# Optimization experiments

Hardware: AMD Instinct MI355X
Metric: run time of the kernel (lower is better)

## Reference

```python
import jax, jax.numpy as jnp
import numpy as np
from jax import lax

B, N, C = 256, 256, 192
HEADS = 6
HD = C // HEADS
WIN = 16
AGENT = 49
POOL = 7            # int(agent_num ** 0.5)
SCALE = HD ** -0.5


def _pool_matrix(inn, out):
    # PyTorch AdaptiveAvgPool2d bin edges: start=floor(i*inn/out), end=ceil((i+1)*inn/out)
    P = np.zeros((out, inn), np.float32)
    for i in range(out):
        s = (i * inn) // out
        e = -(((-(i + 1)) * inn) // out)
        P[i, s:e] = 1.0 / (e - s)
    return jnp.asarray(P)

_P = _pool_matrix(WIN, POOL)  # (7, 16) adaptive-avg-pool operator


def _resize_bilinear(x, out_h, out_w):
    # matches F.interpolate(mode='bilinear', align_corners=False)
    H, W = x.shape[-2], x.shape[-1]
    def idx(out, inn):
        s = (jnp.arange(out, dtype=jnp.float32) + 0.5) * (inn / out) - 0.5
        s = jnp.maximum(s, 0.0)
        i0 = jnp.minimum(jnp.floor(s).astype(jnp.int32), inn - 1)
        i1 = jnp.minimum(i0 + 1, inn - 1)
        return i0, i1, s - i0.astype(jnp.float32)
    h0, h1, th = idx(out_h, H)
    w0, w1, tw = idx(out_w, W)
    xh = x[..., h0, :] * (1.0 - th)[:, None] + x[..., h1, :] * th[:, None]
    return xh[..., :, w0] * (1.0 - tw) + xh[..., :, w1] * tw


def setup_inputs() -> dict:
    key = jax.random.key(0)
    ks = jax.random.split(key, 18)
    lin = lambda k: jax.random.normal(k, (C, C), jnp.float32) * 0.02
    zc = jnp.zeros((C,), jnp.float32)
    tn = lambda k, shp: jax.random.normal(k, shp, jnp.float32) * 0.02
    return {
        "x_F1": jax.random.normal(ks[0], (B, N, C), jnp.float32),
        "x_C2": jax.random.normal(ks[1], (B, N, C), jnp.float32),
        "x_C1": jax.random.normal(ks[2], (B, N, C), jnp.float32),
        "Wq": lin(ks[3]), "bq": zc,
        "Wk": lin(ks[4]), "bk": zc,
        "Wv": lin(ks[5]), "bv": zc,
        "Wa1": lin(ks[6]), "ba1": zc,
        "Wa2": lin(ks[7]), "ba2": zc,
        "an_bias": tn(ks[8], (HEADS, AGENT, 7, 7)),
        "na_bias": tn(ks[9], (HEADS, AGENT, 7, 7)),
        "ah_bias": tn(ks[10], (1, HEADS, AGENT, WIN, 1)),
        "aw_bias": tn(ks[11], (1, HEADS, AGENT, 1, WIN)),
        "ha_bias": tn(ks[12], (1, HEADS, WIN, 1, AGENT)),
        "wa_bias": tn(ks[13], (1, HEADS, 1, WIN, AGENT)),
        "dwc_w": tn(ks[14], (C, 1, 3, 3)),
        "dwc_b": zc,
        "Wp": lin(ks[15]), "bp": zc,
    }


def reference(x_F1, x_C2, x_C1, Wq, bq, Wk, bk, Wv, bv, Wa1, ba1, Wa2, ba2,
              an_bias, na_bias, ah_bias, aw_bias, ha_bias, wa_bias,
              dwc_w, dwc_b, Wp, bp):
    b, n, c = x_F1.shape
    h = w = WIN
    q = x_F1 @ Wq.T + bq
    k = (x_F1 + x_C2 - x_C1) @ Wk.T + bk
    v = (x_C2 - x_C1) @ Wv.T + bv
    # agent tokens: linear -> adaptive avg pool 16x16 -> 7x7 -> (b, 49, c)
    a1 = (x_C1 @ Wa1.T + ba1).reshape(b, h, w, c)
    a1 = jnp.einsum('ph,bhwc,qw->bpqc', _P, a1, _P).reshape(b, AGENT, c)
    a2 = (x_C2 @ Wa2.T + ba2).reshape(b, h, w, c)
    a2 = jnp.einsum('ph,bhwc,qw->bpqc', _P, a2, _P).reshape(b, AGENT, c)
    qh = q.reshape(b, n, HEADS, HD).transpose(0, 2, 1, 3)
    kh = k.reshape(b, n, HEADS, HD).transpose(0, 2, 1, 3)
    vh = v.reshape(b, n, HEADS, HD).transpose(0, 2, 1, 3)
    a1h = a1.reshape(b, AGENT, HEADS, HD).transpose(0, 2, 1, 3)
    a2h = a2.reshape(b, AGENT, HEADS, HD).transpose(0, 2, 1, 3)
    # stage 1: agent <- k/v attention, bias = interp(an_bias) + (ah+aw)
    pb = (_resize_bilinear(an_bias, h, w).reshape(1, HEADS, AGENT, n)
          + (ah_bias + aw_bias).reshape(1, HEADS, AGENT, n))
    attn2 = jax.nn.softmax(SCALE * jnp.einsum('bhad,bhnd->bhan', a2h, kh) + pb, axis=-1)
    agent_v = jnp.einsum('bhan,bhnd->bhad', attn2, vh)
    # stage 2: query <- agent attention, bias = interp(na_bias)^T + (ha+wa)
    ab = (jnp.swapaxes(_resize_bilinear(na_bias, h, w).reshape(HEADS, AGENT, n), -1, -2)[None]
          + (ha_bias + wa_bias).reshape(1, HEADS, n, AGENT))
    q_attn = jax.nn.softmax(SCALE * jnp.einsum('bhnd,bhad->bhna', qh, a1h) + ab, axis=-1)
    x = jnp.einsum('bhna,bhad->bhnd', q_attn, agent_v).transpose(0, 2, 1, 3).reshape(b, n, c)
    # depthwise 3x3 conv on q as spatial map
    q_img = q.reshape(b, h, w, c).transpose(0, 3, 1, 2)
    dw = lax.conv_general_dilated(q_img, dwc_w, (1, 1), ((1, 1), (1, 1)),
                                  feature_group_count=c,
                                  dimension_numbers=('NCHW', 'OIHW', 'NCHW'))
    dw = dw + dwc_b.reshape(1, c, 1, 1)
    x = x + dw.transpose(0, 2, 3, 1).reshape(b, n, c)
    return x @ Wp.T + bp
```

## Files before the change

kernel.cpp:

```cpp
#include <hip/hip_runtime.h>

typedef __bf16 bf16;
typedef __bf16 bf16x8 __attribute__((ext_vector_type(8)));
typedef float  f32x4  __attribute__((ext_vector_type(4)));

#define DEVI __device__ __forceinline__

static constexpr int   BATCH = 256;
static constexpr int   SEQ   = 256;
static constexpr int   CH    = 192;
static constexpr int   NH    = 6;
static constexpr int   AG    = 49;
static constexpr float QK_SCALE = 0.17677669529663687f;

__device__ constexpr int   PPN[16]  = {1,1,2,1,2,1,2,1,1,2,1,2,1,2,1,1};
__device__ constexpr int   PPB0[16] = {0,0,0,1,1,2,2,3,3,3,4,4,5,5,6,6};
__device__ constexpr int   PPB1[16] = {0,0,1,0,2,0,3,0,0,4,0,5,0,6,0,0};
__device__ constexpr float PPW0[16] = {1.f/3.f,1.f/3.f,1.f/3.f,1.f/3.f,1.f/3.f,1.f/3.f,1.f/3.f,0.25f,0.25f,0.25f,
                                       1.f/3.f,1.f/3.f,1.f/3.f,1.f/3.f,1.f/3.f,1.f/3.f};
__device__ constexpr float PPW1[16] = {0.f,0.f,1.f/3.f,0.f,1.f/3.f,0.f,0.25f,0.f,0.f,1.f/3.f,
                                       0.f,1.f/3.f,0.f,1.f/3.f,0.f,0.f};

DEVI float bilin7(const float* m, int i, int j) {
  float sh = (i + 0.5f) * 0.4375f - 0.5f; sh = sh < 0.f ? 0.f : sh;
  float sw = (j + 0.5f) * 0.4375f - 0.5f; sw = sw < 0.f ? 0.f : sw;
  int i0 = (int)sh; if (i0 > 6) i0 = 6;
  int j0 = (int)sw; if (j0 > 6) j0 = 6;
  int i1 = i0 + 1;  if (i1 > 6) i1 = 6;
  int j1 = j0 + 1;  if (j1 > 6) j1 = 6;
  float th = sh - (float)i0, tw = sw - (float)j0;
  float v00 = m[i0*7 + j0], v01 = m[i0*7 + j1];
  float v10 = m[i1*7 + j0], v11 = m[i1*7 + j1];
  return (v00*(1.f-tw) + v01*tw)*(1.f-th) + (v10*(1.f-tw) + v11*tw)*th;
}

__global__ void k_prep(const float* Wq, const float* Wk, const float* Wv,
                       const float* Wa1, const float* Wa2, const float* Wp,
                       const float* an_bias, const float* na_bias,
                       const float* ah_bias, const float* aw_bias,
                       const float* ha_bias, const float* wa_bias,
                       bf16* wsW, float* pb, float* ab, bf16* a1, bf16* a2) {
  int gid = blockIdx.x * 256 + threadIdx.x;
  if (gid < 221184) {
    int mi = gid / 36864, r = gid - mi * 36864;
    const float* W = (mi == 0 ? Wq : mi == 1 ? Wk : mi == 2 ? Wv :
                      mi == 3 ? Wa1 : mi == 4 ? Wa2 : Wp);
    wsW[gid] = (bf16)W[r];
  } else if (gid < 296448) {
    int r = gid - 221184;
    int n = r & 255, ha = r >> 8;
    int i = n >> 4, j = n & 15;
    float val = bilin7(an_bias + (size_t)ha * 49, i, j)
              + ah_bias[ha * 16 + i] + aw_bias[ha * 16 + j];
    pb[r] = val;
  } else if (gid < 371712) {
    int r = gid - 296448;
    int a = r % 49, hn = r / 49;
    int n = hn & 255, hh = hn >> 8;
    int i = n >> 4, j = n & 15;
    float val = bilin7(na_bias + (size_t)(hh * 49 + a) * 49, i, j)
              + ha_bias[(hh * 16 + i) * 49 + a] + wa_bias[(hh * 16 + j) * 49 + a];
    ab[r] = val;
  } else if (gid < 396288) {
    int r = gid - 371712;
    if (r < 12288) a1[(size_t)12544 * CH + r] = (bf16)0.f;
    else           a2[(size_t)12544 * CH + (r - 12288)] = (bf16)0.f;
  }
}

__global__ __launch_bounds__(768, 3) void k_gemm3(
    const float* xF1, const float* xC2, const float* xC1,
    const bf16* wsW, const float* bq, const float* bk, const float* bv,
    bf16* qO, bf16* kO, bf16* vO) {
  __shared__ bf16 sT[3][128][72] __attribute__((aligned(16)));
  const int tid = threadIdx.x, lane = tid & 63, wid = tid >> 6;
  const int l15 = lane & 15, lg = lane >> 4;
  const int job = wid >> 2, quad = wid & 3;
  const int wr = quad >> 1, wc = quad & 1;
  const int m0 = blockIdx.x * 128;

  const bf16*  Wj   = wsW + job * 36864;
  const float* bias = (job == 0) ? bq : (job == 1) ? bk : bv;
  bf16*        outp = (job == 0) ? qO : (job == 1) ? kO : vO;

  f32x4 acc[4][6];
  #pragma unroll
  for (int a = 0; a < 4; ++a)
    #pragma unroll
    for (int b2 = 0; b2 < 6; ++b2) acc[a][b2] = f32x4{0.f, 0.f, 0.f, 0.f};

  const int srow = tid >> 2, qtr = tid & 3;
  const size_t rb = (size_t)(m0 + srow) * CH;

  for (int ks = 0; ks < 3; ++ks) {
    const int k0 = ks * 64;
    if (tid < 512) {
      const int cb = k0 + qtr * 16;
      float4 F[4], A2[4], A1[4];
      const float4* pF = (const float4*)(xF1 + rb + cb);
      const float4* p2 = (const float4*)(xC2 + rb + cb);
      const float4* p1 = (const float4*)(xC1 + rb + cb);
      #pragma unroll
      for (int i = 0; i < 4; ++i) { F[i] = pF[i]; A2[i] = p2[i]; A1[i] = p1[i]; }
      const float* ff = (const float*)F;
      const float* f2 = (const float*)A2;
      const float* f1 = (const float*)A1;
      bf16x8 tq[2], tk[2], tv[2];
      #pragma unroll
      for (int e = 0; e < 16; ++e) {
        const int w = e >> 3, l = e & 7;
        const float xf = ff[e], x2 = f2[e], x1 = f1[e];
        tq[w][l] = (bf16)xf;
        tk[w][l] = (bf16)(xf + x2 - x1);
        tv[w][l] = (bf16)(x2 - x1);
      }
      *(bf16x8*)&sT[0][srow][qtr * 16]     = tq[0];
      *(bf16x8*)&sT[0][srow][qtr * 16 + 8] = tq[1];
      *(bf16x8*)&sT[1][srow][qtr * 16]     = tk[0];
      *(bf16x8*)&sT[1][srow][qtr * 16 + 8] = tk[1];
      *(bf16x8*)&sT[2][srow][qtr * 16]     = tv[0];
      *(bf16x8*)&sT[2][srow][qtr * 16 + 8] = tv[1];
    }
    __syncthreads();
    #pragma unroll
    for (int kk = 0; kk < 64; kk += 32) {
      bf16x8 af[4];
      #pragma unroll
      for (int rt = 0; rt < 4; ++rt)
        af[rt] = *(const bf16x8*)&sT[job][64 * wr + 16 * rt + l15][kk + 8 * lg];
      #pragma unroll
      for (int ct = 0; ct < 6; ++ct) {
        const int ncol = 96 * wc + 16 * ct + l15;
        bf16x8 bfr = *(const bf16x8*)&Wj[(size_t)ncol * CH + k0 + kk + 8 * lg];
        #pragma unroll
        for (int rt = 0; rt < 4; ++rt)
          acc[rt][ct] = __builtin_amdgcn_mfma_f32_16x16x32_bf16(af[rt], bfr, acc[rt][ct], 0, 0, 0);
      }
    }
    __syncthreads();
  }
  #pragma unroll
  for (int ct = 0; ct < 6; ++ct) {
    const int col = 96 * wc + 16 * ct + l15;
    const float bb = bias[col];
    #pragma unroll
    for (int rt = 0; rt < 4; ++rt) {
      const size_t rbase = (size_t)(m0 + 64 * wr + 16 * rt + 4 * lg);
      #pragma unroll
      for (int r = 0; r < 4; ++r)
        outp[(rbase + r) * CH + col] = (bf16)(acc[rt][ct][r] + bb);
    }
  }
}

__global__ __launch_bounds__(192) void k_pool(
    const float* xC1, const float* xC2, bf16* pooled1, bf16* pooled2) {
  const int b = blockIdx.x, which = blockIdx.y, c = threadIdx.x;
  const float* src = (which ? xC2 : xC1) + (size_t)b * SEQ * CH + c;
  bf16* dst = (which ? pooled2 : pooled1) + (size_t)b * AG * CH + c;
  float acc[49];
  #pragma unroll
  for (int a = 0; a < 49; ++a) acc[a] = 0.f;
  #pragma unroll
  for (int i = 0; i < 16; ++i) {
    float jq[7] = {0.f, 0.f, 0.f, 0.f, 0.f, 0.f, 0.f};
    #pragma unroll
    for (int j = 0; j < 16; ++j) {
      const float x = src[(i * 16 + j) * CH];
      jq[PPB0[j]] += PPW0[j] * x;
      if (PPN[j] == 2) jq[PPB1[j]] += PPW1[j] * x;
    }
    {
      const int p0 = PPB0[i]; const float w0 = PPW0[i];
      #pragma unroll
      for (int qq = 0; qq < 7; ++qq) acc[p0 * 7 + qq] += w0 * jq[qq];
    }
    if (PPN[i] == 2) {
      const int p1 = PPB1[i]; const float w1 = PPW1[i];
      #pragma unroll
      for (int qq = 0; qq < 7; ++qq) acc[p1 * 7 + qq] += w1 * jq[qq];
    }
  }
  #pragma unroll
  for (int a = 0; a < 49; ++a) dst[(size_t)a * CH + c] = (bf16)acc[a];
}

template<bool F32OUT>
DEVI void gemm_body(const bf16* Asrc, const bf16* W, const float* bias,
                    void* outp, int m0, bf16 (*sA)[72]) {
  const int tid = threadIdx.x, lane = tid & 63, wid = tid >> 6;
  const int l15 = lane & 15, lg = lane >> 4;
  const int wr = wid >> 1, wc = wid & 1;
  const int srow = tid >> 1, shalf = tid & 1;

  f32x4 acc[4][6];
  #pragma unroll
  for (int a = 0; a < 4; ++a)
    #pragma unroll
    for (int b2 = 0; b2 < 6; ++b2) acc[a][b2] = f32x4{0.f, 0.f, 0.f, 0.f};

  for (int ks = 0; ks < 3; ++ks) {
    const int k0 = ks * 64;
    const uint4* src = (const uint4*)(Asrc + (size_t)(m0 + srow) * CH + k0 + shalf * 32);
    #pragma unroll
    for (int i2 = 0; i2 < 4; ++i2)
      *(uint4*)&sA[srow][shalf * 32 + 8 * i2] = src[i2];
    __syncthreads();
    #pragma unroll
    for (int kk = 0; kk < 64; kk += 32) {
      bf16x8 af[4];
      #pragma unroll
      for (int rt = 0; rt < 4; ++rt)
        af[rt] = *(const bf16x8*)&sA[64 * wr + 16 * rt + l15][kk + 8 * lg];
      #pragma unroll
      for (int ct = 0; ct < 6; ++ct) {
        const int ncol = 96 * wc + 16 * ct + l15;
        bf16x8 bfr = *(const bf16x8*)&W[(size_t)ncol * CH + k0 + kk + 8 * lg];
        #pragma unroll
        for (int rt = 0; rt < 4; ++rt)
          acc[rt][ct] = __builtin_amdgcn_mfma_f32_16x16x32_bf16(af[rt], bfr, acc[rt][ct], 0, 0, 0);
      }
    }
    __syncthreads();
  }
  #pragma unroll
  for (int ct = 0; ct < 6; ++ct) {
    const int col = 96 * wc + 16 * ct + l15;
    const float bb = bias[col];
    #pragma unroll
    for (int rt = 0; rt < 4; ++rt) {
      const size_t rbase = (size_t)(m0 + 64 * wr + 16 * rt + 4 * lg);
      #pragma unroll
      for (int r = 0; r < 4; ++r) {
        float v = acc[rt][ct][r] + bb;
        if (F32OUT) ((float*)outp)[(rbase + r) * CH + col] = v;
        else        ((bf16*)outp)[(rbase + r) * CH + col] = (bf16)v;
      }
    }
  }
}

__global__ __launch_bounds__(256, 2) void k_gemm2(
    const bf16* pooled1, const bf16* pooled2, const bf16* wsW,
    const float* ba1, const float* ba2, bf16* a1, bf16* a2) {
  __shared__ bf16 sA[128][72] __attribute__((aligned(16)));
  const int m0 = blockIdx.x * 128;
  if (blockIdx.y == 0) gemm_body<false>(pooled1, wsW + 3 * 36864, ba1, a1, m0, sA);
  else                 gemm_body<false>(pooled2, wsW + 4 * 36864, ba2, a2, m0, sA);
}

__global__ __launch_bounds__(256, 2) void k_gemm_out(
    const bf16* xsum, const bf16* Wp, const float* bp, float* out) {
  __shared__ bf16 sA[128][72] __attribute__((aligned(16)));
  gemm_body<true>(xsum, Wp, bp, out, blockIdx.x * 128, sA);
}

__global__ __launch_bounds__(256, 2) void k_attn(
    const bf16* q, const bf16* k, const bf16* v,
    const bf16* a1, const bf16* a2, const float* pb, const float* ab,
    bf16* xout) {
  const int h = blockIdx.x, b = blockIdx.y;
  __shared__ char uSmem[36864] __attribute__((aligned(16)));
  bf16 (*log1)[264] = reinterpret_cast<bf16 (*)[264]>(uSmem);
  bf16 (*log2)[72]  = reinterpret_cast<bf16 (*)[72]>(uSmem);
  __shared__ bf16 sVT[32][264] __attribute__((aligned(16)));
  __shared__ bf16 sAVT[32][72] __attribute__((aligned(16)));
  __shared__ float srow1[64];
  __shared__ float srow2[256];

  const int tid = threadIdx.x, lane = tid & 63, wv = tid >> 6;
  const int l15 = lane & 15, lg = lane >> 4;

  const bf16* qb  = q  + (size_t)b * SEQ * CH + h * 32;
  const bf16* kb  = k  + (size_t)b * SEQ * CH + h * 32;
  const bf16* vb  = v  + (size_t)b * SEQ * CH + h * 32;
  const bf16* a1b = a1 + (size_t)b * AG  * CH + h * 32;
  const bf16* a2b = a2 + (size_t)b * AG  * CH + h * 32;

  {
    const int p = tid & 127, dg = tid >> 7;
    const bf16* s0 = vb + (size_t)(2 * p) * CH + dg * 16;
    bf16x8 r0a = ((const bf16x8*)s0)[0];
    bf16x8 r0b = ((const bf16x8*)s0)[1];
    bf16x8 r1a = ((const bf16x8*)(s0 + CH))[0];
    bf16x8 r1b = ((const bf16x8*)(s0 + CH))[1];
    #pragma unroll
    for (int j = 0; j < 8; ++j) {
      union { bf16 e[2]; unsigned u; } u0, u1;
      u0.e[0] = r0a[j]; u0.e[1] = r1a[j];
      u1.e[0] = r0b[j]; u1.e[1] = r1b[j];
      *(unsigned*)&sVT[dg * 16 + j][2 * p]     = u0.u;
      *(unsigned*)&sVT[dg * 16 + 8 + j][2 * p] = u1.u;
    }
  }

  {
    bf16x8 afr[4];
    #pragma unroll
    for (int rt = 0; rt < 4; ++rt)
      afr[rt] = *(const bf16x8*)(a2b + (size_t)(16 * rt + l15) * CH + 8 * lg);
    #pragma unroll
    for (int ct = 0; ct < 4; ++ct) {
      const int n = 64 * wv + 16 * ct + l15;
      bf16x8 bfr = *(const bf16x8*)(kb + (size_t)n * CH + 8 * lg);
      #pragma unroll
      for (int rt = 0; rt < 4; ++rt) {
        f32x4 acc = {0.f, 0.f, 0.f, 0.f};
        acc = __builtin_amdgcn_mfma_f32_16x16x32_bf16(afr[rt], bfr, acc, 0, 0, 0);
        #pragma unroll
        for (int r = 0; r < 4; ++r)
          log1[16 * rt + 4 * lg + r][n] = (bf16)acc[r];
      }
    }
  }
  __syncthreads();

  if (tid < 196) {
    const int a = tid >> 2, qu = tid & 3;
    const float* pbrow = pb + ((size_t)h * AG + a) * SEQ + qu * 64;
    float vbuf[64];
    float m = -1e30f;
    #pragma unroll
    for (int i2 = 0; i2 < 8; ++i2) {
      bf16x8 raw = *(const bf16x8*)&log1[a][qu * 64 + 8 * i2];
      #pragma unroll
      for (int j = 0; j < 8; ++j) {
        float x = QK_SCALE * (float)raw[j] + pbrow[8 * i2 + j];
        vbuf[8 * i2 + j] = x;
        m = fmaxf(m, x);
      }
    }
    m = fmaxf(m, __shfl_xor(m, 1));
    m = fmaxf(m, __shfl_xor(m, 2));
    float s = 0.f;
    #pragma unroll
    for (int i2 = 0; i2 < 8; ++i2) {
      bf16x8 eb;
      #pragma unroll
      for (int j = 0; j < 8; ++j) {
        float e = __expf(vbuf[8 * i2 + j] - m);
        s += e;
        eb[j] = (bf16)e;
      }
      *(bf16x8*)&log1[a][qu * 64 + 8 * i2] = eb;
    }
    s += __shfl_xor(s, 1);
    s += __shfl_xor(s, 2);
    if (qu == 0) srow1[a] = 1.f / s;
  }
  __syncthreads();

  {
    f32x4 acc0 = {0.f, 0.f, 0.f, 0.f}, acc1 = {0.f, 0.f, 0.f, 0.f};
    #pragma unroll
    for (int ksn = 0; ksn < 8; ++ksn) {
      bf16x8 af = *(const bf16x8*)&log1[16 * wv + l15][32 * ksn + 8 * lg];
      bf16x8 b0 = *(const bf16x8*)&sVT[l15][32 * ksn + 8 * lg];
      bf16x8 b1 = *(const bf16x8*)&sVT[16 + l15][32 * ksn + 8 * lg];
      acc0 = __builtin_amdgcn_mfma_f32_16x16x32_bf16(af, b0, acc0, 0, 0, 0);
      acc1 = __builtin_amdgcn_mfma_f32_16x16x32_bf16(af, b1, acc1, 0, 0, 0);
    }
    #pragma unroll
    for (int r = 0; r < 4; ++r) {
      const int a = 16 * wv + 4 * lg + r;
      const float inv = (a < AG) ? srow1[a] : 0.f;
      sAVT[l15][a]      = (bf16)(acc0[r] * inv);
      sAVT[16 + l15][a] = (bf16)(acc1[r] * inv);
    }
  }
  __syncthreads();

  {
    bf16x8 bfr[4];
    #pragma unroll
    for (int ct = 0; ct < 4; ++ct)
      bfr[ct] = *(const bf16x8*)(a1b + (size_t)(16 * ct + l15) * CH + 8 * lg);
    #pragma unroll
    for (int rt = 0; rt < 4; ++rt) {
      bf16x8 af = *(const bf16x8*)(qb + (size_t)(64 * wv + 16 * rt + l15) * CH + 8 * lg);
      #pragma unroll
      for (int ct = 0; ct < 4; ++ct) {
        f32x4 acc = {0.f, 0.f, 0.f, 0.f};
        acc = __builtin_amdgcn_mfma_f32_16x16x32_bf16(af, bfr[ct], acc, 0, 0, 0);
        #pragma unroll
        for (int r = 0; r < 4; ++r)
          log2[64 * wv + 16 * rt + 4 * lg + r][16 * ct + l15] = (bf16)acc[r];
      }
    }
  }
  __syncthreads();

  {
    const float* abrow = ab + ((size_t)h * SEQ + tid) * AG;
    float vb2[49];
    float m = -1e30f;
    #pragma unroll
    for (int i2 = 0; i2 < 6; ++i2) {
      bf16x8 raw = *(const bf16x8*)&log2[tid][8 * i2];
      #pragma unroll
      for (int j = 0; j < 8; ++j) {
        float x = QK_SCALE * (float)raw[j] + abrow[8 * i2 + j];
        vb2[8 * i2 + j] = x;
        m = fmaxf(m, x);
      }
    }
    {
      float x = QK_SCALE * (float)log2[tid][48] + abrow[48];
      vb2[48] = x;
      m = fmaxf(m, x);
    }
    float s = 0.f;
    #pragma unroll
    for (int i2 = 0; i2 < 8; ++i2) {
      bf16x8 eb;
      #pragma unroll
      for (int j = 0; j < 8; ++j) {
        const int idx = 8 * i2 + j;
        float e = 0.f;
        if (idx < AG) { e = __expf(vb2[idx] - m); }
        s += e;
        eb[j] = (bf16)e;
      }
      *(bf16x8*)&log2[tid][8 * i2] = eb;
    }
    srow2[tid] = 1.f / s;
  }
  __syncthreads();

  {
    bf16x8 bfr[2][2];
    #pragma unroll
    for (int ksn = 0; ksn < 2; ++ksn) {
      bfr[ksn][0] = *(const bf16x8*)&sAVT[l15][32 * ksn + 8 * lg];
      bfr[ksn][1] = *(const bf16x8*)&sAVT[16 + l15][32 * ksn + 8 * lg];
    }
    bf16* outp = xout + (size_t)b * SEQ * CH + h * 32;
    #pragma unroll
    for (int rt = 0; rt < 4; ++rt) {
      f32x4 acc0 = {0.f, 0.f, 0.f, 0.f}, acc1 = {0.f, 0.f, 0.f, 0.f};
      #pragma unroll
      for (int ksn = 0; ksn < 2; ++ksn) {
        bf16x8 af = *(const bf16x8*)&log2[64 * wv + 16 * rt + l15][32 * ksn + 8 * lg];
        acc0 = __builtin_amdgcn_mfma_f32_16x16x32_bf16(af, bfr[ksn][0], acc0, 0, 0, 0);
        acc1 = __builtin_amdgcn_mfma_f32_16x16x32_bf16(af, bfr[ksn][1], acc1, 0, 0, 0);
      }
      #pragma unroll
      for (int r = 0; r < 4; ++r) {
        const int nq = 64 * wv + 16 * rt + 4 * lg + r;
        const float inv = srow2[nq];
        outp[(size_t)nq * CH + l15]      = (bf16)(acc0[r] * inv);
        outp[(size_t)nq * CH + 16 + l15] = (bf16)(acc1[r] * inv);
      }
    }
  }
}

DEVI void fma8(float* acc, bf16x8 qv, float4 wa, float4 wb) {
  acc[0] += (float)qv[0] * wa.x; acc[1] += (float)qv[1] * wa.y;
  acc[2] += (float)qv[2] * wa.z; acc[3] += (float)qv[3] * wa.w;
  acc[4] += (float)qv[4] * wb.x; acc[5] += (float)qv[5] * wb.y;
  acc[6] += (float)qv[6] * wb.z; acc[7] += (float)qv[7] * wb.w;
}

__global__ __launch_bounds__(256) void k_dwconv(
    const bf16* q, const bf16* xattn, const float* dwc_w, const float* dwc_b,
    bf16* xsum) {
  __shared__ bf16 sQ[144][200] __attribute__((aligned(16)));
  __shared__ float sW[9][192] __attribute__((aligned(16)));
  const int half = blockIdx.x, b = blockIdx.y;
  const int t = threadIdx.x;
  const int base_n = half ? 112 : 0;

  if (t < 144) {
    const bf16* qs = q + ((size_t)b * SEQ + base_n + t) * CH;
    #pragma unroll
    for (int i2 = 0; i2 < 24; ++i2)
      *(uint4*)&sQ[t][8 * i2] = ((const uint4*)qs)[i2];
  }
  for (int idx = t; idx < 9 * 192; idx += 256) {
    int cc = idx / 9, tap = idx - cc * 9;
    sW[tap][cc] = dwc_w[idx];
  }
  __syncthreads();

  const int nloc = t & 127, chalf = t >> 7;
  const int n = half * 128 + nloc;
  const int ii = n >> 4, jj = n & 15;
  const bf16* xa = xattn + ((size_t)b * SEQ + n) * CH;
  bf16* xo = xsum + ((size_t)b * SEQ + n) * CH;
  const int c_base = chalf * 96;

  for (int c0 = c_base; c0 < c_base + 96; c0 += 8) {
    float accv[8];
    {
      const float4* bsrc = (const float4*)(dwc_b + c0);
      float4 b0 = bsrc[0], b1 = bsrc[1];
      accv[0] = b0.x; accv[1] = b0.y; accv[2] = b0.z; accv[3] = b0.w;
      accv[4] = b1.x; accv[5] = b1.y; accv[6] = b1.z; accv[7] = b1.w;
    }
    {
      bf16x8 xv = *(const bf16x8*)(xa + c0);
      #pragma unroll
      for (int j = 0; j < 8; ++j) accv[j] += (float)xv[j];
    }
    #pragma unroll
    for (int di = 0; di < 3; ++di) {
      const int i2 = ii + di - 1;
      if ((unsigned)i2 >= 16u) continue;
      #pragma unroll
      for (int dj = 0; dj < 3; ++dj) {
        const int j2 = jj + dj - 1;
        if ((unsigned)j2 >= 16u) continue;
        const int nn = i2 * 16 + j2 - base_n;
        bf16x8 qv = *(const bf16x8*)&sQ[nn][c0];
        const float4* wv4 = (const float4*)&sW[di * 3 + dj][c0];
        fma8(accv, qv, wv4[0], wv4[1]);
      }
    }
    bf16x8 ob;
    #pragma unroll
    for (int j = 0; j < 8; ++j) ob[j] = (bf16)accv[j];
    *(bf16x8*)(xo + c0) = ob;
  }
}

extern "C" void kernel_launch(void* const* d_in, const int* in_sizes, int n_in,
                              void* d_out, int out_size, void* d_ws, size_t ws_size,
                              hipStream_t stream) {
  (void)in_sizes; (void)n_in; (void)out_size; (void)ws_size;
  const float* xF1 = (const float*)d_in[0];
  const float* xC2 = (const float*)d_in[1];
  const float* xC1 = (const float*)d_in[2];
  const float* Wq  = (const float*)d_in[3];
  const float* bq  = (const float*)d_in[4];
  const float* Wk  = (const float*)d_in[5];
  const float* bk  = (const float*)d_in[6];
  const float* Wv  = (const float*)d_in[7];
  const float* bv  = (const float*)d_in[8];
  const float* Wa1 = (const float*)d_in[9];
  const float* ba1 = (const float*)d_in[10];
  const float* Wa2 = (const float*)d_in[11];
  const float* ba2 = (const float*)d_in[12];
  const float* an_bias = (const float*)d_in[13];
  const float* na_bias = (const float*)d_in[14];
  const float* ah_bias = (const float*)d_in[15];
  const float* aw_bias = (const float*)d_in[16];
  const float* ha_bias = (const float*)d_in[17];
  const float* wa_bias = (const float*)d_in[18];
  const float* dwc_w = (const float*)d_in[19];
  const float* dwc_b = (const float*)d_in[20];
  const float* Wp  = (const float*)d_in[21];
  const float* bp  = (const float*)d_in[22];

  char* ws = (char*)d_ws;
  size_t off = 0;
  auto nxt = [&](size_t bytes) -> char* {
    char* p = ws + off;
    off = (off + bytes + 255) & ~(size_t)255;
    return p;
  };
  const size_t XSZ = (size_t)BATCH * SEQ * CH;
  const size_t ASZ = ((size_t)BATCH * AG + 64) * CH;

  bf16*  wsW     = (bf16*)nxt(6 * 36864 * sizeof(bf16));
  float* pb      = (float*)nxt(6 * 49 * 256 * sizeof(float));
  float* ab      = (float*)nxt(6 * 256 * 49 * sizeof(float));
  bf16*  pooled1 = (bf16*)nxt(ASZ * sizeof(bf16));
  bf16*  pooled2 = (bf16*)nxt(ASZ * sizeof(bf16));
  bf16*  qB      = (bf16*)nxt(XSZ * sizeof(bf16));
  bf16*  kB      = (bf16*)nxt(XSZ * sizeof(bf16));
  bf16*  vB      = (bf16*)nxt(XSZ * sizeof(bf16));
  bf16*  a1B     = (bf16*)nxt(ASZ * sizeof(bf16));
  bf16*  a2B     = (bf16*)nxt(ASZ * sizeof(bf16));
  bf16*  xattn   = (bf16*)nxt(XSZ * sizeof(bf16));
  bf16*  xsum    = (bf16*)nxt(XSZ * sizeof(bf16));

  k_prep<<<1548, 256, 0, stream>>>(Wq, Wk, Wv, Wa1, Wa2, Wp,
                                   an_bias, na_bias, ah_bias, aw_bias,
                                   ha_bias, wa_bias, wsW, pb, ab, a1B, a2B);
  k_gemm3<<<512, 768, 0, stream>>>(xF1, xC2, xC1, wsW, bq, bk, bv, qB, kB, vB);
  k_pool<<<dim3(BATCH, 2), 192, 0, stream>>>(xC1, xC2, pooled1, pooled2);
  k_gemm2<<<dim3(98, 2), 256, 0, stream>>>(pooled1, pooled2, wsW, ba1, ba2, a1B, a2B);
  k_attn<<<dim3(NH, BATCH), 256, 0, stream>>>(qB, kB, vB, a1B, a2B, pb, ab, xattn);
  k_dwconv<<<dim3(2, BATCH), 256, 0, stream>>>(qB, xattn, dwc_w, dwc_b, xsum);
  k_gemm_out<<<512, 256, 0, stream>>>(xsum, wsW + 5 * 36864, bp, (float*)d_out);
}
```

Measured before the change: 247.3 us.

## Retile QKV and output GEMMs to 32-row blocks with staged coalesced stores

The fused QKV projection drops from 128-row blocks of 768 threads to 32-row blocks of 256 threads. Each block loads the full K into shared memory once, loops over the three projections, and writes results back through shared memory as coalesced vector stores. The output projection gets the same 32-row retiling and stages its fp32 results in shared memory so stores are contiguous. The pooling kernel now splits rows across two thread halves, reads float2 values and reduces through shared memory, and the QKV launch is moved after pooling. The aim is more blocks for better occupancy and coalesced global writes, at the cost of less weight reuse per block.

Result: slower. 312.0 us (+26.2%).

```diff
diff --git a/kernel.cpp b/kernel.cpp
--- a/kernel.cpp
+++ b/kernel.cpp
@@ -68,126 +68,150 @@
   }
 }
 
-__global__ __launch_bounds__(768, 3) void k_gemm3(
+__global__ __launch_bounds__(192) void k_pool(
+    const float* xC1, const float* xC2, bf16* pooled1, bf16* pooled2) {
+  __shared__ float lred[7][192];
+  const int b = blockIdx.x, which = blockIdx.y, t = threadIdx.x;
+  const int c2 = t % 96, ih = t / 96;
+  const float* src = (which ? xC2 : xC1) + (size_t)b * SEQ * CH + 2 * c2;
+  bf16* dst = (which ? pooled2 : pooled1) + (size_t)b * AG * CH + 2 * c2;
+
+  float accx[4][7], accy[4][7];
+  #pragma unroll
+  for (int p = 0; p < 4; ++p)
+    #pragma unroll
+    for (int q = 0; q < 7; ++q) { accx[p][q] = 0.f; accy[p][q] = 0.f; }
+
+  #pragma unroll
+  for (int il = 0; il < 8; ++il) {
+    const int i = ih * 8 + il;
+    float jqx[7] = {0,0,0,0,0,0,0}, jqy[7] = {0,0,0,0,0,0,0};
+    #pragma unroll
+    for (int j = 0; j < 16; ++j) {
+      float2 x = *(const float2*)(src + (size_t)(i * 16 + j) * CH);
+      jqx[PPB0[j]] += PPW0[j] * x.x;  jqy[PPB0[j]] += PPW0[j] * x.y;
+      if (PPN[j] == 2) { jqx[PPB1[j]] += PPW1[j] * x.x;  jqy[PPB1[j]] += PPW1[j] * x.y; }
+    }
+    const int p0 = PPB0[i] - 3 * ih;
+    const float w0 = PPW0[i];
+    #pragma unroll
+    for (int q = 0; q < 7; ++q) { accx[p0][q] += w0 * jqx[q]; accy[p0][q] += w0 * jqy[q]; }
+    if (PPN[i] == 2) {
+      const int p1 = PPB1[i] - 3 * ih;
+      const float w1 = PPW1[i];
+      #pragma unroll
+      for (int q = 0; q < 7; ++q) { accx[p1][q] += w1 * jqx[q]; accy[p1][q] += w1 * jqy[q]; }
+    }
+  }
+  if (ih == 1) {
+    #pragma unroll
+    for (int q = 0; q < 7; ++q) {
+      lred[q][2 * c2] = accx[0][q]; lred[q][2 * c2 + 1] = accy[0][q];
+    }
+  }
+  __syncthreads();
+  if (ih == 0) {
+    #pragma unroll
+    for (int q = 0; q < 7; ++q) {
+      accx[3][q] += lred[q][2 * c2]; accy[3][q] += lred[q][2 * c2 + 1];
+    }
+  }
+  const int lp0 = ih ? 1 : 0, np = ih ? 3 : 4, gb = ih ? 4 : 0;
+  for (int lp = 0; lp < np; ++lp) {
+    #pragma unroll
+    for (int q = 0; q < 7; ++q) {
+      const int a = (gb + lp) * 7 + q;
+      union { bf16 e[2]; unsigned u; } u;
+      u.e[0] = (bf16)accx[lp0 + lp][q];
+      u.e[1] = (bf16)accy[lp0 + lp][q];
+      *(unsigned*)&dst[(size_t)a * CH] = u.u;
+    }
+  }
+}
+
+__global__ __launch_bounds__(256, 4) void k_gemm3(
     const float* xF1, const float* xC2, const float* xC1,
     const bf16* wsW, const float* bq, const float* bk, const float* bv,
     bf16* qO, bf16* kO, bf16* vO) {
-  __shared__ bf16 sT[3][128][72] __attribute__((aligned(16)));
+  __shared__ bf16 sT[3][32][200] __attribute__((aligned(16)));
   const int tid = threadIdx.x, lane = tid & 63, wid = tid >> 6;
   const int l15 = lane & 15, lg = lane >> 4;
-  const int job = wid >> 2, quad = wid & 3;
-  const int wr = quad >> 1, wc = quad & 1;
-  const int m0 = blockIdx.x * 128;
-
-  const bf16*  Wj   = wsW + job * 36864;
-  const float* bias = (job == 0) ? bq : (job == 1) ? bk : bv;
-  bf16*        outp = (job == 0) ? qO : (job == 1) ? kO : vO;
-
-  f32x4 acc[4][6];
-  #pragma unroll
-  for (int a = 0; a < 4; ++a)
-    #pragma unroll
-    for (int b2 = 0; b2 < 6; ++b2) acc[a][b2] = f32x4{0.f, 0.f, 0.f, 0.f};
-
-  const int srow = tid >> 2, qtr = tid & 3;
-  const size_t rb = (size_t)(m0 + srow) * CH;
-
-  for (int ks = 0; ks < 3; ++ks) {
-    const int k0 = ks * 64;
-    if (tid < 512) {
-      const int cb = k0 + qtr * 16;
-      float4 F[4], A2[4], A1[4];
-      const float4* pF = (const float4*)(xF1 + rb + cb);
-      const float4* p2 = (const float4*)(xC2 + rb + cb);
-      const float4* p1 = (const float4*)(xC1 + rb + cb);
-      #pragma unroll
-      for (int i = 0; i < 4; ++i) { F[i] = pF[i]; A2[i] = p2[i]; A1[i] = p1[i]; }
-      const float* ff = (const float*)F;
-      const float* f2 = (const float*)A2;
-      const float* f1 = (const float*)A1;
-      bf16x8 tq[2], tk[2], tv[2];
-      #pragma unroll
-      for (int e = 0; e < 16; ++e) {
-        const int w = e >> 3, l = e & 7;
-        const float xf = ff[e], x2 = f2[e], x1 = f1[e];
-        tq[w][l] = (bf16)xf;
-        tk[w][l] = (bf16)(xf + x2 - x1);
-        tv[w][l] = (bf16)(x2 - x1);
-      }
-      *(bf16x8*)&sT[0][srow][qtr * 16]     = tq[0];
-      *(bf16x8*)&sT[0][srow][qtr * 16 + 8] = tq[1];
-      *(bf16x8*)&sT[1][srow][qtr * 16]     = tk[0];
-      *(bf16x8*)&sT[1][srow][qtr * 16 + 8] = tk[1];
-      *(bf16x8*)&sT[2][srow][qtr * 16]     = tv[0];
-      *(bf16x8*)&sT[2][srow][qtr * 16 + 8] = tv[1];
+  const int m0 = blockIdx.x * 32;
+  const int srow = tid >> 3, chunk = tid & 7;
+
+  {
+    const size_t rb = (size_t)(m0 + srow) * CH + chunk * 24;
+    const float4* pF = (const float4*)(xF1 + rb);
+    const float4* p2 = (const float4*)(xC2 + rb);
+    const float4* p1 = (const float4*)(xC1 + rb);
+    #pragma unroll
+    for (int g = 0; g < 3; ++g) {
+      float ff[8], f2[8], f1[8];
+      *(float4*)&ff[0] = pF[2 * g]; *(float4*)&ff[4] = pF[2 * g + 1];
+      *(float4*)&f2[0] = p2[2 * g]; *(float4*)&f2[4] = p2[2 * g + 1];
+      *(float4*)&f1[0] = p1[2 * g]; *(float4*)&f1[4] = p1[2 * g + 1];
+      bf16x8 tq, tk, tv;
+      #pragma unroll
+      for (int e = 0; e < 8; ++e) {
+        const float d = f2[e] - f1[e];
+        tq[e] = (bf16)ff[e];
+        tk[e] = (bf16)(ff[e] + d);
+        tv[e] = (bf16)d;
+      }
+      *(bf16x8*)&sT[0][srow][chunk * 24 + 8 * g] = tq;
+      *(bf16x8*)&sT[1][srow][chunk * 24 + 8 * g] = tk;
+      *(bf16x8*)&sT[2][srow][chunk * 24 + 8 * g] = tv;
+    }
+  }
+  __syncthreads();
+
+  #pragma unroll 1
+  for (int job = 0; job < 3; ++job) {
+    const bf16*  Wj   = wsW + job * 36864;
+    const float* bias = (job == 0) ? bq : (job == 1) ? bk : bv;
+    bf16*        outp = (job == 0) ? qO : (job == 1) ? kO : vO;
+
+    f32x4 acc[2][3];
+    #pragma unroll
+    for (int rt = 0; rt < 2; ++rt)
+      #pragma unroll
+      for (int ct = 0; ct < 3; ++ct) acc[rt][ct] = f32x4{0.f, 0.f, 0.f, 0.f};
+
+    #pragma unroll
+    for (int kk = 0; kk < 6; ++kk) {
+      bf16x8 af0 = *(const bf16x8*)&sT[job][l15][kk * 32 + 8 * lg];
+      bf16x8 af1 = *(const bf16x8*)&sT[job][16 + l15][kk * 32 + 8 * lg];
+      #pragma unroll
+      for (int ct = 0; ct < 3; ++ct) {
+        const int ncol = 48 * wid + 16 * ct + l15;
+        bf16x8 bfr = *(const bf16x8*)&Wj[(size_t)ncol * CH + kk * 32 + 8 * lg];
+        acc[0][ct] = __builtin_amdgcn_mfma_f32_16x16x32_bf16(af0, bfr, acc[0][ct], 0, 0, 0);
+        acc[1][ct] = __builtin_amdgcn_mfma_f32_16x16x32_bf16(af1, bfr, acc[1][ct], 0, 0, 0);
+      }
     }
     __syncthreads();
     #pragma unroll
-    for (int kk = 0; kk < 64; kk += 32) {
-      bf16x8 af[4];
-      #pragma unroll
-      for (int rt = 0; rt < 4; ++rt)
-        af[rt] = *(const bf16x8*)&sT[job][64 * wr + 16 * rt + l15][kk + 8 * lg];
-      #pragma unroll
-      for (int ct = 0; ct < 6; ++ct) {
-        const int ncol = 96 * wc + 16 * ct + l15;
-        bf16x8 bfr = *(const bf16x8*)&Wj[(size_t)ncol * CH + k0 + kk + 8 * lg];
+    for (int ct = 0; ct < 3; ++ct) {
+      const int col = 48 * wid + 16 * ct + l15;
+      const float bb = bias[col];
+      #pragma unroll
+      for (int rt = 0; rt < 2; ++rt)
         #pragma unroll
-        for (int rt = 0; rt < 4; ++rt)
-          acc[rt][ct] = __builtin_amdgcn_mfma_f32_16x16x32_bf16(af[rt], bfr, acc[rt][ct], 0, 0, 0);
-      }
+        for (int r = 0; r < 4; ++r)
+          sT[job][16 * rt + 4 * lg + r][col] = (bf16)(acc[rt][ct][r] + bb);
     }
     __syncthreads();
-  }
-  #pragma unroll
-  for (int ct = 0; ct < 6; ++ct) {
-    const int col = 96 * wc + 16 * ct + l15;
-    const float bb = bias[col];
-    #pragma unroll
-    for (int rt = 0; rt < 4; ++rt) {
-      const size_t rbase = (size_t)(m0 + 64 * wr + 16 * rt + 4 * lg);
-      #pragma unroll
-      for (int r = 0; r < 4; ++r)
-        outp[(rbase + r) * CH + col] = (bf16)(acc[rt][ct][r] + bb);
-    }
-  }
-}
-
-__global__ __launch_bounds__(192) void k_pool(
-    const float* xC1, const float* xC2, bf16* pooled1, bf16* pooled2) {
-  const int b = blockIdx.x, which = blockIdx.y, c = threadIdx.x;
-  const float* src = (which ? xC2 : xC1) + (size_t)b * SEQ * CH + c;
-  bf16* dst = (which ? pooled2 : pooled1) + (size_t)b * AG * CH + c;
-  float acc[49];
-  #pragma unroll
-  for (int a = 0; a < 49; ++a) acc[a] = 0.f;
-  #pragma unroll
-  for (int i = 0; i < 16; ++i) {
-    float jq[7] = {0.f, 0.f, 0.f, 0.f, 0.f, 0.f, 0.f};
-    #pragma unroll
-    for (int j = 0; j < 16; ++j) {
-      const float x = src[(i * 16 + j) * CH];
-      jq[PPB0[j]] += PPW0[j] * x;
-      if (PPN[j] == 2) jq[PPB1[j]] += PPW1[j] * x;
-    }
     {
-      const int p0 = PPB0[i]; const float w0 = PPW0[i];
-      #pragma unroll
-      for (int qq = 0; qq < 7; ++qq) acc[p0 * 7 + qq] += w0 * jq[qq];
-    }
-    if (PPN[i] == 2) {
-      const int p1 = PPB1[i]; const float w1 = PPW1[i];
-      #pragma unroll
-      for (int qq = 0; qq < 7; ++qq) acc[p1 * 7 + qq] += w1 * jq[qq];
-    }
-  }
-  #pragma unroll
-  for (int a = 0; a < 49; ++a) dst[(size_t)a * CH + c] = (bf16)acc[a];
-}
-
-template<bool F32OUT>
+      bf16* orow = outp + (size_t)(m0 + srow) * CH + chunk * 24;
+      #pragma unroll
+      for (int g = 0; g < 3; ++g)
+        *(bf16x8*)&orow[8 * g] = *(const bf16x8*)&sT[job][srow][chunk * 24 + 8 * g];
+    }
+  }
+}
+
 DEVI void gemm_body(const bf16* Asrc, const bf16* W, const float* bias,
-                    void* outp, int m0, bf16 (*sA)[72]) {
+                    bf16* outp, int m0, bf16 (*sA)[72]) {
   const int tid = threadIdx.x, lane = tid & 63, wid = tid >> 6;
   const int l15 = lane & 15, lg = lane >> 4;
   const int wr = wid >> 1, wc = wid & 1;
@@ -231,11 +255,8 @@
     for (int rt = 0; rt < 4; ++rt) {
       const size_t rbase = (size_t)(m0 + 64 * wr + 16 * rt + 4 * lg);
       #pragma unroll
-      for (int r = 0; r < 4; ++r) {
-        float v = acc[rt][ct][r] + bb;
-        if (F32OUT) ((float*)outp)[(rbase + r) * CH + col] = v;
-        else        ((bf16*)outp)[(rbase + r) * CH + col] = (bf16)v;
-      }
+      for (int r = 0; r < 4; ++r)
+        outp[(rbase + r) * CH + col] = (bf16)(acc[rt][ct][r] + bb);
     }
   }
 }
@@ -245,14 +266,64 @@
     const float* ba1, const float* ba2, bf16* a1, bf16* a2) {
   __shared__ bf16 sA[128][72] __attribute__((aligned(16)));
   const int m0 = blockIdx.x * 128;
-  if (blockIdx.y == 0) gemm_body<false>(pooled1, wsW + 3 * 36864, ba1, a1, m0, sA);
-  else                 gemm_body<false>(pooled2, wsW + 4 * 36864, ba2, a2, m0, sA);
-}
-
-__global__ __launch_bounds__(256, 2) void k_gemm_out(
+  if (blockIdx.y == 0) gemm_body(pooled1, wsW + 3 * 36864, ba1, a1, m0, sA);
+  else                 gemm_body(pooled2, wsW + 4 * 36864, ba2, a2, m0, sA);
+}
+
+__global__ __launch_bounds__(256, 4) void k_gemm_out(
     const bf16* xsum, const bf16* Wp, const float* bp, float* out) {
-  __shared__ bf16 sA[128][72] __attribute__((aligned(16)));
-  gemm_body<true>(xsum, Wp, bp, out, blockIdx.x * 128, sA);
+  __shared__ char smem[25088] __attribute__((aligned(16)));
+  bf16  (*sA)[200] = reinterpret_cast<bf16 (*)[200]>(smem);
+  float (*sO)[196] = reinterpret_cast<float (*)[196]>(smem);
+  const int tid = threadIdx.x, lane = tid & 63, wid = tid >> 6;
+  const int l15 = lane & 15, lg = lane >> 4;
+  const int m0 = blockIdx.x * 32;
+  const int srow = tid >> 3, chunk = tid & 7;
+
+  {
+    const bf16* arow = xsum + (size_t)(m0 + srow) * CH + chunk * 24;
+    #pragma unroll
+    for (int g = 0; g < 3; ++g)
+      *(bf16x8*)&sA[srow][chunk * 24 + 8 * g] = *(const bf16x8*)&arow[8 * g];
+  }
+  __syncthreads();
+
+  f32x4 acc[2][3];
+  #pragma unroll
+  for (int rt = 0; rt < 2; ++rt)
+    #pragma unroll
+    for (int ct = 0; ct < 3; ++ct) acc[rt][ct] = f32x4{0.f, 0.f, 0.f, 0.f};
+
+  #pragma unroll
+  for (int kk = 0; kk < 6; ++kk) {
+    bf16x8 af0 = *(const bf16x8*)&sA[l15][kk * 32 + 8 * lg];
+    bf16x8 af1 = *(const bf16x8*)&sA[16 + l15][kk * 32 + 8 * lg];
+    #pragma unroll
+    for (int ct = 0; ct < 3; ++ct) {
+      const int ncol = 48 * wid + 16 * ct + l15;
+      bf16x8 bfr = *(const bf16x8*)&Wp[(size_t)ncol * CH + kk * 32 + 8 * lg];
+      acc[0][ct] = __builtin_amdgcn_mfma_f32_16x16x32_bf16(af0, bfr, acc[0][ct], 0, 0, 0);
+      acc[1][ct] = __builtin_amdgcn_mfma_f32_16x16x32_bf16(af1, bfr, acc[1][ct], 0, 0, 0);
+    }
+  }
+  __syncthreads();
+  #pragma unroll
+  for (int ct = 0; ct < 3; ++ct) {
+    const int col = 48 * wid + 16 * ct + l15;
+    const float bb = bp[col];
+    #pragma unroll
+    for (int rt = 0; rt < 2; ++rt)
+      #pragma unroll
+      for (int r = 0; r < 4; ++r)
+        sO[16 * rt + 4 * lg + r][col] = acc[rt][ct][r] + bb;
+  }
+  __syncthreads();
+  {
+    float* orow = out + (size_t)(m0 + srow) * CH + chunk * 24;
+    #pragma unroll
+    for (int g = 0; g < 6; ++g)
+      *(float4*)&orow[4 * g] = *(const float4*)&sO[srow][chunk * 24 + 4 * g];
+  }
 }
 
 __global__ __launch_bounds__(256, 2) void k_attn(
@@ -578,10 +649,10 @@
   k_prep<<<1548, 256, 0, stream>>>(Wq, Wk, Wv, Wa1, Wa2, Wp,
                                    an_bias, na_bias, ah_bias, aw_bias,
                                    ha_bias, wa_bias, wsW, pb, ab, a1B, a2B);
-  k_gemm3<<<512, 768, 0, stream>>>(xF1, xC2, xC1, wsW, bq, bk, bv, qB, kB, vB);
   k_pool<<<dim3(BATCH, 2), 192, 0, stream>>>(xC1, xC2, pooled1, pooled2);
   k_gemm2<<<dim3(98, 2), 256, 0, stream>>>(pooled1, pooled2, wsW, ba1, ba2, a1B, a2B);
+  k_gemm3<<<2048, 256, 0, stream>>>(xF1, xC2, xC1, wsW, bq, bk, bv, qB, kB, vB);
   k_attn<<<dim3(NH, BATCH), 256, 0, stream>>>(qB, kB, vB, a1B, a2B, pb, ab, xattn);
   k_dwconv<<<dim3(2, BATCH), 256, 0, stream>>>(qB, xattn, dwc_w, dwc_b, xsum);
-  k_gemm_out<<<512, 256, 0, stream>>>(xsum, wsW + 5 * 36864, bp, (float*)d_out);
-}
+  k_gemm_out<<<2048, 256, 0, stream>>>(xsum, wsW + 5 * 36864, bp, (float*)d_out);
+}
```

## Split QKV input conversion into a separate pass and load GEMM tiles via global-to-LDS

Applied to the files above, without the earlier changes.

The fused fp32-to-bf16 conversion plus QKV GEMM is split into a streaming conversion kernel that writes XOR-swizzled bf16 rows, followed by a per-job GEMM grid that loads the whole 128x192 A tile with global_load_lds and stages its output through LDS for coalesced stores. The output projection GEMM uses the same direct-to-LDS single-shot load, reading a swizzled xsum produced by the dwconv kernel. Workspace buffers are reused for xattn and xsum. This adds an extra bf16 round trip through global memory for the converted inputs, traded against fewer barriers, cheaper LDS fills and better store coalescing.

New measurement: 248.6 us. No clear change (+0.5%).

```diff
diff --git a/kernel.cpp b/kernel.cpp
--- a/kernel.cpp
+++ b/kernel.cpp
@@ -20,6 +20,23 @@
                                        1.f/3.f,1.f/3.f,1.f/3.f,1.f/3.f,1.f/3.f,1.f/3.f};
 __device__ constexpr float PPW1[16] = {0.f,0.f,1.f/3.f,0.f,1.f/3.f,0.f,0.25f,0.f,0.f,1.f/3.f,
                                        0.f,1.f/3.f,0.f,1.f/3.f,0.f,0.f};
+
+#if defined(__has_builtin)
+#if __has_builtin(__builtin_amdgcn_global_load_lds)
+#define HAVE_GLL 1
+#endif
+#endif
+
+DEVI void gll16(const void* g, void* l, int lane) {
+#ifdef HAVE_GLL
+  (void)lane;
+  __builtin_amdgcn_global_load_lds(
+      (const __attribute__((address_space(1))) void*)g,
+      (__attribute__((address_space(3))) void*)l, 16, 0, 0);
+#else
+  *(uint4*)((char*)l + lane * 16) = *(const uint4*)((const char*)g);
+#endif
+}
 
 DEVI float bilin7(const float* m, int i, int j) {
   float sh = (i + 0.5f) * 0.4375f - 0.5f; sh = sh < 0.f ? 0.f : sh;
@@ -68,88 +85,36 @@
   }
 }
 
-__global__ __launch_bounds__(768, 3) void k_gemm3(
+__global__ __launch_bounds__(256) void k_combo(
     const float* xF1, const float* xC2, const float* xC1,
-    const bf16* wsW, const float* bq, const float* bk, const float* bv,
-    bf16* qO, bf16* kO, bf16* vO) {
-  __shared__ bf16 sT[3][128][72] __attribute__((aligned(16)));
-  const int tid = threadIdx.x, lane = tid & 63, wid = tid >> 6;
-  const int l15 = lane & 15, lg = lane >> 4;
-  const int job = wid >> 2, quad = wid & 3;
-  const int wr = quad >> 1, wc = quad & 1;
-  const int m0 = blockIdx.x * 128;
-
-  const bf16*  Wj   = wsW + job * 36864;
-  const float* bias = (job == 0) ? bq : (job == 1) ? bk : bv;
-  bf16*        outp = (job == 0) ? qO : (job == 1) ? kO : vO;
-
-  f32x4 acc[4][6];
-  #pragma unroll
-  for (int a = 0; a < 4; ++a)
-    #pragma unroll
-    for (int b2 = 0; b2 < 6; ++b2) acc[a][b2] = f32x4{0.f, 0.f, 0.f, 0.f};
-
-  const int srow = tid >> 2, qtr = tid & 3;
-  const size_t rb = (size_t)(m0 + srow) * CH;
-
-  for (int ks = 0; ks < 3; ++ks) {
-    const int k0 = ks * 64;
-    if (tid < 512) {
-      const int cb = k0 + qtr * 16;
-      float4 F[4], A2[4], A1[4];
-      const float4* pF = (const float4*)(xF1 + rb + cb);
-      const float4* p2 = (const float4*)(xC2 + rb + cb);
-      const float4* p1 = (const float4*)(xC1 + rb + cb);
-      #pragma unroll
-      for (int i = 0; i < 4; ++i) { F[i] = pF[i]; A2[i] = p2[i]; A1[i] = p1[i]; }
-      const float* ff = (const float*)F;
-      const float* f2 = (const float*)A2;
-      const float* f1 = (const float*)A1;
-      bf16x8 tq[2], tk[2], tv[2];
-      #pragma unroll
-      for (int e = 0; e < 16; ++e) {
-        const int w = e >> 3, l = e & 7;
-        const float xf = ff[e], x2 = f2[e], x1 = f1[e];
-        tq[w][l] = (bf16)xf;
-        tk[w][l] = (bf16)(xf + x2 - x1);
-        tv[w][l] = (bf16)(x2 - x1);
-      }
-      *(bf16x8*)&sT[0][srow][qtr * 16]     = tq[0];
-      *(bf16x8*)&sT[0][srow][qtr * 16 + 8] = tq[1];
-      *(bf16x8*)&sT[1][srow][qtr * 16]     = tk[0];
-      *(bf16x8*)&sT[1][srow][qtr * 16 + 8] = tk[1];
-      *(bf16x8*)&sT[2][srow][qtr * 16]     = tv[0];
-      *(bf16x8*)&sT[2][srow][qtr * 16 + 8] = tv[1];
-    }
-    __syncthreads();
-    #pragma unroll
-    for (int kk = 0; kk < 64; kk += 32) {
-      bf16x8 af[4];
-      #pragma unroll
-      for (int rt = 0; rt < 4; ++rt)
-        af[rt] = *(const bf16x8*)&sT[job][64 * wr + 16 * rt + l15][kk + 8 * lg];
-      #pragma unroll
-      for (int ct = 0; ct < 6; ++ct) {
-        const int ncol = 96 * wc + 16 * ct + l15;
-        bf16x8 bfr = *(const bf16x8*)&Wj[(size_t)ncol * CH + k0 + kk + 8 * lg];
-        #pragma unroll
-        for (int rt = 0; rt < 4; ++rt)
-          acc[rt][ct] = __builtin_amdgcn_mfma_f32_16x16x32_bf16(af[rt], bfr, acc[rt][ct], 0, 0, 0);
-      }
-    }
-    __syncthreads();
-  }
-  #pragma unroll
-  for (int ct = 0; ct < 6; ++ct) {
-    const int col = 96 * wc + 16 * ct + l15;
-    const float bb = bias[col];
-    #pragma unroll
-    for (int rt = 0; rt < 4; ++rt) {
-      const size_t rbase = (size_t)(m0 + 64 * wr + 16 * rt + 4 * lg);
-      #pragma unroll
-      for (int r = 0; r < 4; ++r)
-        outp[(rbase + r) * CH + col] = (bf16)(acc[rt][ct][r] + bb);
-    }
+    bf16* f1b, bf16* kin, bf16* vin) {
+  const int base = blockIdx.x * 768;
+  #pragma unroll
+  for (int s = 0; s < 3; ++s) {
+    const int slot = base + threadIdx.x + 256 * s;
+    const int row  = slot / 24;
+    const int cb   = slot - row * 24;
+    const size_t rf = (size_t)row * CH + cb * 8;
+    float f[8], c2[8], c1[8];
+    *(float4*)&f[0]  = *(const float4*)(xF1 + rf);
+    *(float4*)&f[4]  = *(const float4*)(xF1 + rf + 4);
+    *(float4*)&c2[0] = *(const float4*)(xC2 + rf);
+    *(float4*)&c2[4] = *(const float4*)(xC2 + rf + 4);
+    *(float4*)&c1[0] = *(const float4*)(xC1 + rf);
+    *(float4*)&c1[4] = *(const float4*)(xC1 + rf + 4);
+    bf16x8 tq, tk, tv;
+    #pragma unroll
+    for (int e = 0; e < 8; ++e) {
+      const float d = c2[e] - c1[e];
+      tq[e] = (bf16)f[e];
+      tk[e] = (bf16)(f[e] + d);
+      tv[e] = (bf16)d;
+    }
+    const size_t rowb = (size_t)row * 384;
+    const int    byt  = (cb * 16) ^ ((row & 7) << 4);
+    *(bf16x8*)((char*)f1b + rowb + byt) = tq;
+    *(bf16x8*)((char*)kin + rowb + byt) = tk;
+    *(bf16x8*)((char*)vin + rowb + byt) = tv;
   }
 }
 
@@ -185,9 +150,80 @@
   for (int a = 0; a < 49; ++a) dst[(size_t)a * CH + c] = (bf16)acc[a];
 }
 
-template<bool F32OUT>
+__global__ __launch_bounds__(256, 3) void k_gemm3b(
+    const bf16* f1b, const bf16* kin, const bf16* vin, const bf16* wsW,
+    const float* bq, const float* bk, const float* bv,
+    bf16* qO, bf16* kO, bf16* vO) {
+  __shared__ char sA[49152] __attribute__((aligned(16)));
+  const int tid = threadIdx.x, lane = tid & 63, wid = tid >> 6;
+  const int l15 = lane & 15, lg = lane >> 4;
+  const int wr = wid >> 1, wc = wid & 1;
+  const int job = blockIdx.y;
+  const int m0 = blockIdx.x * 128;
+  const bf16*  Aj   = (job == 0 ? f1b : job == 1 ? kin : vin);
+  const bf16*  Wj   = wsW + job * 36864;
+  const float* bias = (job == 0 ? bq : job == 1 ? bk : bv);
+  bf16*        outp = (job == 0 ? qO : job == 1 ? kO : vO);
+
+  {
+    const char* gsrc = (const char*)Aj + (size_t)m0 * 384;
+    #pragma unroll
+    for (int i = 0; i < 12; ++i) {
+      const int off = (wid * 12 + i) * 1024;
+      gll16(gsrc + off + lane * 16, sA + off, lane);
+    }
+  }
+  __syncthreads();
+
+  f32x4 acc[4][6];
+  #pragma unroll
+  for (int a = 0; a < 4; ++a)
+    #pragma unroll
+    for (int b2 = 0; b2 < 6; ++b2) acc[a][b2] = f32x4{0.f, 0.f, 0.f, 0.f};
+
+  #pragma unroll
+  for (int kk = 0; kk < 6; ++kk) {
+    bf16x8 af[4];
+    #pragma unroll
+    for (int rt = 0; rt < 4; ++rt) {
+      const int row = 64 * wr + 16 * rt + l15;
+      af[rt] = *(const bf16x8*)(sA + row * 384 + ((kk * 64 + lg * 16) ^ ((row & 7) << 4)));
+    }
+    #pragma unroll
+    for (int ct = 0; ct < 6; ++ct) {
+      const int ncol = 96 * wc + 16 * ct + l15;
+      bf16x8 bfr = *(const bf16x8*)&Wj[(size_t)ncol * CH + kk * 32 + 8 * lg];
+      #pragma unroll
+      for (int rt = 0; rt < 4; ++rt)
+        acc[rt][ct] = __builtin_amdgcn_mfma_f32_16x16x32_bf16(af[rt], bfr, acc[rt][ct], 0, 0, 0);
+    }
+  }
+  __syncthreads();
+  #pragma unroll
+  for (int ct = 0; ct < 6; ++ct) {
+    const int col = 96 * wc + 16 * ct + l15;
+    const float bb = bias[col];
+    #pragma unroll
+    for (int rt = 0; rt < 4; ++rt)
+      #pragma unroll
+      for (int r = 0; r < 4; ++r) {
+        const int row = 64 * wr + 16 * rt + 4 * lg + r;
+        *(bf16*)(sA + row * 384 + ((2 * col) ^ ((row & 7) << 4))) = (bf16)(acc[rt][ct][r] + bb);
+      }
+  }
+  __syncthreads();
+  #pragma unroll
+  for (int g = 0; g < 12; ++g) {
+    const int ch  = tid + 256 * g;
+    const int row = ch / 24;
+    const int y   = (ch - row * 24) * 16;
+    bf16x8 vv = *(const bf16x8*)(sA + row * 384 + (y ^ ((row & 7) << 4)));
+    *(bf16x8*)((char*)outp + (size_t)(m0 + row) * 384 + y) = vv;
+  }
+}
+
 DEVI void gemm_body(const bf16* Asrc, const bf16* W, const float* bias,
-                    void* outp, int m0, bf16 (*sA)[72]) {
+                    bf16* outp, int m0, bf16 (*sA)[72]) {
   const int tid = threadIdx.x, lane = tid & 63, wid = tid >> 6;
   const int l15 = lane & 15, lg = lane >> 4;
   const int wr = wid >> 1, wc = wid & 1;
@@ -231,11 +267,8 @@
     for (int rt = 0; rt < 4; ++rt) {
       const size_t rbase = (size_t)(m0 + 64 * wr + 16 * rt + 4 * lg);
       #pragma unroll
-      for (int r = 0; r < 4; ++r) {
-        float v = acc[rt][ct][r] + bb;
-        if (F32OUT) ((float*)outp)[(rbase + r) * CH + col] = v;
-        else        ((bf16*)outp)[(rbase + r) * CH + col] = (bf16)v;
-      }
+      for (int r = 0; r < 4; ++r)
+        outp[(rbase + r) * CH + col] = (bf16)(acc[rt][ct][r] + bb);
     }
   }
 }
@@ -245,14 +278,61 @@
     const float* ba1, const float* ba2, bf16* a1, bf16* a2) {
   __shared__ bf16 sA[128][72] __attribute__((aligned(16)));
   const int m0 = blockIdx.x * 128;
-  if (blockIdx.y == 0) gemm_body<false>(pooled1, wsW + 3 * 36864, ba1, a1, m0, sA);
-  else                 gemm_body<false>(pooled2, wsW + 4 * 36864, ba2, a2, m0, sA);
-}
-
-__global__ __launch_bounds__(256, 2) void k_gemm_out(
+  if (blockIdx.y == 0) gemm_body(pooled1, wsW + 3 * 36864, ba1, a1, m0, sA);
+  else                 gemm_body(pooled2, wsW + 4 * 36864, ba2, a2, m0, sA);
+}
+
+__global__ __launch_bounds__(256, 3) void k_gemm_out(
     const bf16* xsum, const bf16* Wp, const float* bp, float* out) {
-  __shared__ bf16 sA[128][72] __attribute__((aligned(16)));
-  gemm_body<true>(xsum, Wp, bp, out, blockIdx.x * 128, sA);
+  __shared__ char sA[49152] __attribute__((aligned(16)));
+  const int tid = threadIdx.x, lane = tid & 63, wid = tid >> 6;
+  const int l15 = lane & 15, lg = lane >> 4;
+  const int wr = wid >> 1, wc = wid & 1;
+  const int m0 = blockIdx.x * 128;
+
+  {
+    const char* gsrc = (const char*)xsum + (size_t)m0 * 384;
+    #pragma unroll
+    for (int i = 0; i < 12; ++i) {
+      const int off = (wid * 12 + i) * 1024;
+      gll16(gsrc + off + lane * 16, sA + off, lane);
+    }
+  }
+  __syncthreads();
+
+  f32x4 acc[4][6];
+  #pragma unroll
+  for (int a = 0; a < 4; ++a)
+    #pragma unroll
+    for (int b2 = 0; b2 < 6; ++b2) acc[a][b2] = f32x4{0.f, 0.f, 0.f, 0.f};
+
+  #pragma unroll
+  for (int kk = 0; kk < 6; ++kk) {
+    bf16x8 af[4];
+    #pragma unroll
+    for (int rt = 0; rt < 4; ++rt) {
+      const int row = 64 * wr + 16 * rt + l15;
+      af[rt] = *(const bf16x8*)(sA + row * 384 + ((kk * 64 + lg * 16) ^ ((row & 7) << 4)));
+    }
+    #pragma unroll
+    for (int ct = 0; ct < 6; ++ct) {
+      const int ncol = 96 * wc + 16 * ct + l15;
+      bf16x8 bfr = *(const bf16x8*)&Wp[(size_t)ncol * CH + kk * 32 + 8 * lg];
+      #pragma unroll
+      for (int rt = 0; rt < 4; ++rt)
+        acc[rt][ct] = __builtin_amdgcn_mfma_f32_16x16x32_bf16(af[rt], bfr, acc[rt][ct], 0, 0, 0);
+    }
+  }
+  #pragma unroll
+  for (int ct = 0; ct < 6; ++ct) {
+    const int col = 96 * wc + 16 * ct + l15;
+    const float bb = bp[col];
+    #pragma unroll
+    for (int rt = 0; rt < 4; ++rt)
+      #pragma unroll
+      for (int r = 0; r < 4; ++r)
+        out[(size_t)(m0 + 64 * wr + 16 * rt + 4 * lg + r) * CH + col] = acc[rt][ct][r] + bb;
+  }
 }
 
 __global__ __launch_bounds__(256, 2) void k_attn(
@@ -487,7 +567,8 @@
   const int n = half * 128 + nloc;
   const int ii = n >> 4, jj = n & 15;
   const bf16* xa = xattn + ((size_t)b * SEQ + n) * CH;
-  bf16* xo = xsum + ((size_t)b * SEQ + n) * CH;
+  char* xo = (char*)(xsum + ((size_t)b * SEQ + n) * CH);
+  const int sw = (n & 7) << 4;
   const int c_base = chalf * 96;
 
   for (int c0 = c_base; c0 < c_base + 96; c0 += 8) {
@@ -520,7 +601,7 @@
     bf16x8 ob;
     #pragma unroll
     for (int j = 0; j < 8; ++j) ob[j] = (bf16)accv[j];
-    *(bf16x8*)(xo + c0) = ob;
+    *(bf16x8*)(xo + ((2 * c0) ^ sw)) = ob;
   }
 }
 
@@ -567,18 +648,22 @@
   float* ab      = (float*)nxt(6 * 256 * 49 * sizeof(float));
   bf16*  pooled1 = (bf16*)nxt(ASZ * sizeof(bf16));
   bf16*  pooled2 = (bf16*)nxt(ASZ * sizeof(bf16));
+  bf16*  f1b     = (bf16*)nxt(XSZ * sizeof(bf16));
+  bf16*  kin     = (bf16*)nxt(XSZ * sizeof(bf16));
+  bf16*  vin     = (bf16*)nxt(XSZ * sizeof(bf16));
   bf16*  qB      = (bf16*)nxt(XSZ * sizeof(bf16));
   bf16*  kB      = (bf16*)nxt(XSZ * sizeof(bf16));
   bf16*  vB      = (bf16*)nxt(XSZ * sizeof(bf16));
   bf16*  a1B     = (bf16*)nxt(ASZ * sizeof(bf16));
   bf16*  a2B     = (bf16*)nxt(ASZ * sizeof(bf16));
-  bf16*  xattn   = (bf16*)nxt(XSZ * sizeof(bf16));
-  bf16*  xsum    = (bf16*)nxt(XSZ * sizeof(bf16));
+  bf16*  xattn   = f1b;
+  bf16*  xsum    = kin;
 
   k_prep<<<1548, 256, 0, stream>>>(Wq, Wk, Wv, Wa1, Wa2, Wp,
                                    an_bias, na_bias, ah_bias, aw_bias,
                                    ha_bias, wa_bias, wsW, pb, ab, a1B, a2B);
-  k_gemm3<<<512, 768, 0, stream>>>(xF1, xC2, xC1, wsW, bq, bk, bv, qB, kB, vB);
+  k_combo<<<2048, 256, 0, stream>>>(xF1, xC2, xC1, f1b, kin, vin);
+  k_gemm3b<<<dim3(512, 3), 256, 0, stream>>>(f1b, kin, vin, wsW, bq, bk, bv, qB, kB, vB);
   k_pool<<<dim3(BATCH, 2), 192, 0, stream>>>(xC1, xC2, pooled1, pooled2);
   k_gemm2<<<dim3(98, 2), 256, 0, stream>>>(pooled1, pooled2, wsW, ba1, ba2, a1B, a2B);
   k_attn<<<dim3(NH, BATCH), 256, 0, stream>>>(qB, kB, vB, a1B, a2B, pb, ab, xattn);
```
